# Optimization experiments

Measured on AMD Instinct MI355X. Metric: run time of the kernel, lower is better.

## Reference

```python
import jax, jax.numpy as jnp
import numpy as np


def setup_inputs() -> dict:
    key = jax.random.key(0)
    k1, k2, k3, k4, k5 = jax.random.split(key, 5)
    return {
        "d1": jax.random.normal(k1, (2, 4096, 512), dtype=jnp.float32),
        "d2": jax.random.normal(k2, (2, 512, 4096), dtype=jnp.float32),
        "d3": jax.random.normal(k3, (2, 4096, 512), dtype=jnp.float32),
        "d4": jax.random.normal(k4, (512, 512), dtype=jnp.float32),
        "d5": jax.random.normal(k5, (1, 512), dtype=jnp.float32),
    }


def reference(d1, d2, d3, d4, d5):
    # attention core: scores = d1 @ d2 -> [2, 4096, 4096]
    scores = jnp.einsum('bsd,bdt->bst', d1, d2)
    attn = jax.nn.softmax(scores, axis=2)
    # weighted values: [2, 4096, 512]
    ctx = jnp.einsum('bst,btd->bsd', attn, d3)
    # flatten batch*seq and apply final projection with bias (addmm)
    x = ctx.reshape(8192, 512)
    return d5 + x @ d4  # d5 [1,512] broadcasts over rows
```

## Files before the change

### kernel.cpp

```cpp
#include <hip/hip_runtime.h>

typedef unsigned short u16;
typedef __attribute__((ext_vector_type(8))) short short8;
typedef __attribute__((ext_vector_type(4))) float f32x4;

#define MFMA16(a, b, c) __builtin_amdgcn_mfma_f32_16x16x32_bf16((a), (b), (c), 0, 0, 0)
#define ASYNC_CP16(g, l)                                                        \
  __builtin_amdgcn_global_load_lds((const __attribute__((address_space(1))) void*)(g), \
                                   (__attribute__((address_space(3))) void*)(l), 16, 0, 0)

constexpr int Bb = 2, Ss = 4096, Tt = 4096, Dd = 512;
constexpr int BM = 64, BN = 64, TP = 4;
constexpr int TPART = Tt / TP;
constexpr int TCH = TPART / BN;

constexpr size_t SZ_BF = (size_t)Bb * Ss * Dd * 2;
constexpr size_t O_QH   = 0;
constexpr size_t O_QL   = O_QH + SZ_BF;
constexpr size_t O_D2TH = O_QL + SZ_BF;
constexpr size_t O_D2TL = O_D2TH + SZ_BF;
constexpr size_t O_D3T  = O_D2TL + SZ_BF;
constexpr size_t O_D4T  = O_D3T + SZ_BF;
constexpr size_t O_CTX  = O_D4T + (size_t)512 * 512 * 2;
constexpr size_t O_OP   = O_CTX + SZ_BF;
constexpr size_t O_MP   = O_OP + (size_t)TP * SZ_BF;
constexpr size_t O_LP   = O_MP + (size_t)TP * Bb * Ss * 4;

__device__ __forceinline__ u16 f2bf(float x) {
  union { float f; unsigned u; } v; v.f = x;
  unsigned r = v.u + 0x7fffu + ((v.u >> 16) & 1u);
  return (u16)(r >> 16);
}
__device__ __forceinline__ float bf2f(u16 h) {
  union { unsigned u; float f; } v; v.u = ((unsigned)h) << 16;
  return v.f;
}

__device__ __forceinline__ void transpose_sp(const float* __restrict__ in,
                                             u16* __restrict__ outh,
                                             u16* __restrict__ outl, int R, int C,
                                             int bx, int by, int bz,
                                             int tx, int ty, float* tile) {
  const float* inb = in + (size_t)bz * R * C;
  const int x = bx * 32 + tx;
  const int y0 = by * 32;
  for (int j = ty; j < 32; j += 8)
    tile[j * 33 + tx] = inb[(size_t)(y0 + j) * C + x];
  __syncthreads();
  const size_t ob = (size_t)bz * C * R;
  for (int j = ty; j < 32; j += 8) {
    float v = tile[tx * 33 + j];
    size_t oi = ob + (size_t)(bx * 32 + j) * R + (y0 + tx);
    u16 h = f2bf(v);
    outh[oi] = h;
    if (outl) outl[oi] = f2bf(v - bf2f(h));
  }
}

__global__ void prep_kernel(const float* __restrict__ d1, const float* __restrict__ d2,
                            const float* __restrict__ d3, const float* __restrict__ d4,
                            u16* __restrict__ qh, u16* __restrict__ ql,
                            u16* __restrict__ d2th, u16* __restrict__ d2tl,
                            u16* __restrict__ d3t, u16* __restrict__ d4t) {
  __shared__ float tile[32 * 33];
  const int bid = blockIdx.x;
  const int tid = threadIdx.x;
  const int tx = tid & 31, ty = tid >> 5;
  if (bid < 4096) {
    const int i = bid * 256 + tid;
    float4 v = ((const float4*)d1)[i];
    ushort4 hh, ll;
    hh.x = f2bf(v.x); ll.x = f2bf(v.x - bf2f(hh.x));
    hh.y = f2bf(v.y); ll.y = f2bf(v.y - bf2f(hh.y));
    hh.z = f2bf(v.z); ll.z = f2bf(v.z - bf2f(hh.z));
    hh.w = f2bf(v.w); ll.w = f2bf(v.w - bf2f(hh.w));
    ((ushort4*)qh)[i] = hh;
    ((ushort4*)ql)[i] = ll;
  } else if (bid < 8192) {
    const int t = bid - 4096;
    transpose_sp(d2, d2th, d2tl, 512, 4096, t & 127, (t >> 7) & 15, t >> 11, tx, ty, tile);
  } else if (bid < 12288) {
    const int t = bid - 8192;
    transpose_sp(d3, d3t, nullptr, 4096, 512, t & 15, (t >> 4) & 127, t >> 11, tx, ty, tile);
  } else {
    const int t = bid - 12288;
    transpose_sp(d4, d4t, nullptr, 512, 512, t & 15, t >> 4, 0, tx, ty, tile);
  }
}

__global__ __launch_bounds__(256, 2)
void flash_part_kernel(const u16* __restrict__ qh_g,
                       const u16* __restrict__ ql_g,
                       const u16* __restrict__ d2th,
                       const u16* __restrict__ d2tl,
                       const u16* __restrict__ d3t,
                       u16* __restrict__ opart,
                       float* __restrict__ mpart,
                       float* __restrict__ lpart) {
  __shared__ u16 bufs[2][16384];
  __shared__ u16 ph[64 * 72];

  const int tid = threadIdx.x;
  const int wave = tid >> 6, lane = tid & 63, quad = lane >> 4, l15 = lane & 15;
  const int m0 = wave * 16;
  const int s0 = blockIdx.x * BM, tp = blockIdx.y, b = blockIdx.z;

  f32x4 o_acc[32];
#pragma unroll
  for (int i = 0; i < 32; i++) o_acc[i] = (f32x4){0.f, 0.f, 0.f, 0.f};
  f32x4 s_acc[4];
  float m_r[4] = {-INFINITY, -INFINITY, -INFINITY, -INFINITY};
  float l_r[4] = {0.f, 0.f, 0.f, 0.f};

  const u16* qh_row = qh_g + ((size_t)b * Ss + s0 + m0 + l15) * Dd + quad * 8;
  const u16* ql_row = ql_g + ((size_t)b * Ss + s0 + m0 + l15) * Dd + quad * 8;
  const u16* kh_b = d2th + (size_t)b * Tt * Dd;
  const u16* kl_b = d2tl + (size_t)b * Tt * Dd;
  const u16* v_b  = d3t  + (size_t)b * Dd * Tt;

  const int l4 = lane >> 4;
  const int cb16 = lane & 15;
  const int vr8 = lane >> 3;
  const int vcb = (lane & 7) ^ (vr8 & 7);

  {
    const int t0 = tp * TPART;
#pragma unroll
    for (int u = 0; u < 4; u++) {
      const int rloc = wave * 16 + u * 4 + l4;
      const int gb = cb16 ^ (u * 4 + l4);
      const u16* sh = kh_b + (size_t)(t0 + rloc) * Dd + gb * 8;
      const u16* sl = kl_b + (size_t)(t0 + rloc) * Dd + gb * 8;
      u16* ld = &bufs[0][(wave * 16 + u * 4) * 128];
      ASYNC_CP16(sh, ld);
      ASYNC_CP16(sl, ld + 8192);
    }
  }
  __syncthreads();

  for (int tc = 0; tc < TCH; tc++) {
#pragma unroll
    for (int sub = 0; sub < 8; sub++) {
      const bool has_next = (sub < 7) || (tc < TCH - 1);
      const int nsub = (sub + 1) & 7;
      const int ntc = (sub == 7) ? tc + 1 : tc;

      if (has_next) {
        const int nt0 = tp * TPART + ntc * BN;
        u16* nb = bufs[nsub & 1];
        if (nsub < 4) {
          const int d0 = nsub * 128;
#pragma unroll
          for (int u = 0; u < 4; u++) {
            const int rloc = wave * 16 + u * 4 + l4;
            const int gb = cb16 ^ (u * 4 + l4);
            const u16* sh = kh_b + (size_t)(nt0 + rloc) * Dd + d0 + gb * 8;
            const u16* sl = kl_b + (size_t)(nt0 + rloc) * Dd + d0 + gb * 8;
            u16* ld = &nb[(wave * 16 + u * 4) * 128];
            ASYNC_CP16(sh, ld);
            ASYNC_CP16(sl, ld + 8192);
          }
        } else {
          const int nc = nsub - 4;
#pragma unroll
          for (int u = 0; u < 4; u++) {
            const int rloc = wave * 32 + u * 8 + vr8;
            const u16* sv = v_b + (size_t)(nc * 128 + rloc) * Tt + nt0 + vcb * 8;
            u16* ld = &nb[(wave * 32 + u * 8) * 64];
            ASYNC_CP16(sv, ld);
          }
        }
      }

      const u16* bb = bufs[sub & 1];
      if (sub < 4) {
        if (sub == 0) {
#pragma unroll
          for (int nt = 0; nt < 4; nt++) s_acc[nt] = (f32x4){0.f, 0.f, 0.f, 0.f};
        }
        const int d0 = sub * 128;
        short8 ah[4], al[4];
#pragma unroll
        for (int ks = 0; ks < 4; ks++) {
          ah[ks] = *(const short8*)(qh_row + d0 + ks * 32);
          al[ks] = *(const short8*)(ql_row + d0 + ks * 32);
        }
#pragma unroll
        for (int ks = 0; ks < 4; ks++) {
#pragma unroll
          for (int nt = 0; nt < 4; nt++) {
            const int rr = nt * 16 + l15;
            const int off = rr * 128 + (((ks * 4 + quad) ^ l15)) * 8;
            short8 bh = *(const short8*)&bb[off];
            short8 bl = *(const short8*)&bb[8192 + off];
            s_acc[nt] = MFMA16(ah[ks], bh, s_acc[nt]);
            s_acc[nt] = MFMA16(al[ks], bh, s_acc[nt]);
            s_acc[nt] = MFMA16(ah[ks], bl, s_acc[nt]);
          }
        }
        if (sub == 3) {
          float alpha[4], psum[4];
#pragma unroll
          for (int r = 0; r < 4; r++) {
            float v = fmaxf(fmaxf(s_acc[0][r], s_acc[1][r]), fmaxf(s_acc[2][r], s_acc[3][r]));
            v = fmaxf(v, __shfl_xor(v, 1));
            v = fmaxf(v, __shfl_xor(v, 2));
            v = fmaxf(v, __shfl_xor(v, 4));
            v = fmaxf(v, __shfl_xor(v, 8));
            float mn = fmaxf(m_r[r], v);
            alpha[r] = __expf(m_r[r] - mn);
            m_r[r] = mn;
            psum[r] = 0.f;
          }
#pragma unroll
          for (int nt = 0; nt < 4; nt++) {
#pragma unroll
            for (int r = 0; r < 4; r++) {
              float p = __expf(s_acc[nt][r] - m_r[r]);
              psum[r] += p;
              ph[(m0 + quad * 4 + r) * 72 + nt * 16 + l15] = f2bf(p);
            }
          }
#pragma unroll
          for (int r = 0; r < 4; r++) {
            float v = psum[r];
            v += __shfl_xor(v, 1);
            v += __shfl_xor(v, 2);
            v += __shfl_xor(v, 4);
            v += __shfl_xor(v, 8);
            l_r[r] = l_r[r] * alpha[r] + v;
          }
          bool need = (alpha[0] != 1.f) | (alpha[1] != 1.f) | (alpha[2] != 1.f) | (alpha[3] != 1.f);
          if (__any(need)) {
#pragma unroll
            for (int j = 0; j < 32; j++)
#pragma unroll
              for (int r = 0; r < 4; r++) o_acc[j][r] *= alpha[r];
          }
        }
      } else {
        const int nc = sub - 4;
#pragma unroll
        for (int ks = 0; ks < 2; ks++) {
          const int kk = ks * 32 + quad * 8;
          short8 ap = *(const short8*)&ph[(m0 + l15) * 72 + kk];
#pragma unroll
          for (int nt = 0; nt < 8; nt++) {
            const int rr = nt * 16 + l15;
            const int off = rr * 64 + (((ks * 4 + quad) ^ (l15 & 7))) * 8;
            short8 bv = *(const short8*)&bb[off];
            o_acc[nc * 8 + nt] = MFMA16(ap, bv, o_acc[nc * 8 + nt]);
          }
        }
      }

      __syncthreads();
    }
  }

  const size_t obase = (((size_t)tp * Bb + b) * Ss + s0) * Dd;
#pragma unroll
  for (int j = 0; j < 32; j++) {
    const int col = (j >> 3) * 128 + (j & 7) * 16 + l15;
#pragma unroll
    for (int r = 0; r < 4; r++) {
      const int row = m0 + quad * 4 + r;
      opart[obase + (size_t)row * Dd + col] = f2bf(o_acc[j][r]);
    }
  }
  if (l15 == 0) {
    const size_t sbase = ((size_t)tp * Bb + b) * Ss + s0;
#pragma unroll
    for (int r = 0; r < 4; r++) {
      const int row = m0 + quad * 4 + r;
      mpart[sbase + row] = m_r[r];
      lpart[sbase + row] = l_r[r];
    }
  }
}

__global__ void combine_kernel(const u16* __restrict__ opart,
                               const float* __restrict__ mpart,
                               const float* __restrict__ lpart,
                               u16* __restrict__ ctx) {
  const int idx = blockIdx.x * blockDim.x + threadIdx.x;
  const int vpr = Dd / 8;
  const int row = idx / vpr;
  const int dv = (idx % vpr) * 8;
  float mv[TP], mM = -INFINITY;
#pragma unroll
  for (int p = 0; p < TP; p++) {
    mv[p] = mpart[(size_t)p * Bb * Ss + row];
    mM = fmaxf(mM, mv[p]);
  }
  float w[TP], denom = 0.f;
#pragma unroll
  for (int p = 0; p < TP; p++) {
    float e = __expf(mv[p] - mM);
    w[p] = e;
    denom += e * lpart[(size_t)p * Bb * Ss + row];
  }
  const float inv = 1.0f / denom;
  float acc[8];
#pragma unroll
  for (int e = 0; e < 8; e++) acc[e] = 0.f;
#pragma unroll
  for (int p = 0; p < TP; p++) {
    uint4 raw = *(const uint4*)&opart[(size_t)p * Bb * Ss * Dd + (size_t)row * Dd + dv];
    const u16* u = (const u16*)&raw;
#pragma unroll
    for (int e = 0; e < 8; e++) acc[e] += w[p] * bf2f(u[e]);
  }
  u16 outv[8];
#pragma unroll
  for (int e = 0; e < 8; e++) outv[e] = f2bf(acc[e] * inv);
  *(uint4*)&ctx[(size_t)row * Dd + dv] = *(const uint4*)outv;
}

__global__ __launch_bounds__(256, 2)
void proj_kernel(const u16* __restrict__ ctx,
                 const u16* __restrict__ d4t,
                 const float* __restrict__ d5,
                 float* __restrict__ out) {
  __shared__ u16 a_lds[128 * 40], b_lds[128 * 40];
  const int tid = threadIdx.x;
  const int wave = tid >> 6, lane = tid & 63, quad = lane >> 4, l15 = lane & 15;
  const int m0w = (wave & 1) * 64, n0w = (wave >> 1) * 64;
  const int bm = blockIdx.x, bn = blockIdx.y;
  f32x4 acc[4][4];
#pragma unroll
  for (int i = 0; i < 4; i++)
#pragma unroll
    for (int j = 0; j < 4; j++) acc[i][j] = (f32x4){0.f, 0.f, 0.f, 0.f};

  const int srow = tid >> 2, scol = (tid & 3) * 8;
  for (int kt = 0; kt < 16; kt++) {
    const int k0 = kt * 32;
    __syncthreads();
#pragma unroll
    for (int pass = 0; pass < 2; pass++) {
      const int row = srow + pass * 64;
      *(uint4*)&a_lds[row * 40 + scol] =
          *(const uint4*)&ctx[(size_t)(bm * 128 + row) * Dd + k0 + scol];
      *(uint4*)&b_lds[row * 40 + scol] =
          *(const uint4*)&d4t[(size_t)(bn * 128 + row) * Dd + k0 + scol];
    }
    __syncthreads();
    short8 af[4], bfr[4];
#pragma unroll
    for (int i = 0; i < 4; i++)
      af[i] = *(const short8*)&a_lds[(m0w + 16 * i + l15) * 40 + quad * 8];
#pragma unroll
    for (int j = 0; j < 4; j++)
      bfr[j] = *(const short8*)&b_lds[(n0w + 16 * j + l15) * 40 + quad * 8];
#pragma unroll
    for (int i = 0; i < 4; i++)
#pragma unroll
      for (int j = 0; j < 4; j++) acc[i][j] = MFMA16(af[i], bfr[j], acc[i][j]);
  }
#pragma unroll
  for (int j = 0; j < 4; j++) {
    const int colg = bn * 128 + n0w + 16 * j + l15;
    const float bias = d5[colg];
#pragma unroll
    for (int i = 0; i < 4; i++) {
#pragma unroll
      for (int r = 0; r < 4; r++) {
        const int rowg = bm * 128 + m0w + 16 * i + quad * 4 + r;
        out[(size_t)rowg * 512 + colg] = acc[i][j][r] + bias;
      }
    }
  }
}

extern "C" void kernel_launch(void* const* d_in, const int* in_sizes, int n_in,
                              void* d_out, int out_size, void* d_ws, size_t ws_size,
                              hipStream_t stream) {
  (void)in_sizes; (void)n_in; (void)out_size; (void)ws_size;
  const float* d1 = (const float*)d_in[0];
  const float* d2 = (const float*)d_in[1];
  const float* d3 = (const float*)d_in[2];
  const float* d4 = (const float*)d_in[3];
  const float* d5 = (const float*)d_in[4];
  float* out = (float*)d_out;
  char* ws = (char*)d_ws;

  u16* qh_g = (u16*)(ws + O_QH);
  u16* ql_g = (u16*)(ws + O_QL);
  u16* d2th = (u16*)(ws + O_D2TH);
  u16* d2tl = (u16*)(ws + O_D2TL);
  u16* d3t  = (u16*)(ws + O_D3T);
  u16* d4t  = (u16*)(ws + O_D4T);
  u16* ctx  = (u16*)(ws + O_CTX);
  u16* opart = (u16*)(ws + O_OP);
  float* mpart = (float*)(ws + O_MP);
  float* lpart = (float*)(ws + O_LP);

  prep_kernel<<<12544, 256, 0, stream>>>(d1, d2, d3, d4, qh_g, ql_g, d2th, d2tl, d3t, d4t);
  flash_part_kernel<<<dim3(Ss / BM, TP, Bb), 256, 0, stream>>>(qh_g, ql_g, d2th, d2tl, d3t,
                                                               opart, mpart, lpart);
  combine_kernel<<<(Bb * Ss * Dd / 8) / 256, 256, 0, stream>>>(opart, mpart, lpart, ctx);
  proj_kernel<<<dim3(64, 4), 256, 0, stream>>>(ctx, d4t, d5, out);
}
```

Before: 555.7 us.

## Double query tile to 128 rows with 8 waves and hoist Q fragments into registers

The flash attention partial kernel now uses 128 query rows per block with 512 threads. Each staged K/V tile in shared memory is therefore shared by twice as many waves, and each wave issues half as many async copies. The query hi/lo fragments for all of D are loaded once into registers instead of being re-read from global memory on every chunk. The grid is reordered so the T-partition and batch are the fast index. This costs many more registers per thread (32 extra short8 values on top of 32 f32x4 accumulators), which risks spilling or lower occupancy at launch bounds of 512 threads and 2 blocks, and it halves the number of blocks.

```diff
diff --git a/kernel.cpp b/kernel.cpp
--- a/kernel.cpp
+++ b/kernel.cpp
@@ -10,7 +10,7 @@
                                    (__attribute__((address_space(3))) void*)(l), 16, 0, 0)
 
 constexpr int Bb = 2, Ss = 4096, Tt = 4096, Dd = 512;
-constexpr int BM = 64, BN = 64, TP = 4;
+constexpr int BM = 128, BN = 64, TP = 4;
 constexpr int TPART = Tt / TP;
 constexpr int TCH = TPART / BN;
 
@@ -88,7 +88,7 @@
   }
 }
 
-__global__ __launch_bounds__(256, 2)
+__global__ __launch_bounds__(512, 2)
 void flash_part_kernel(const u16* __restrict__ qh_g,
                        const u16* __restrict__ ql_g,
                        const u16* __restrict__ d2th,
@@ -98,12 +98,13 @@
                        float* __restrict__ mpart,
                        float* __restrict__ lpart) {
   __shared__ u16 bufs[2][16384];
-  __shared__ u16 ph[64 * 72];
+  __shared__ u16 ph[128 * 72];
 
   const int tid = threadIdx.x;
   const int wave = tid >> 6, lane = tid & 63, quad = lane >> 4, l15 = lane & 15;
   const int m0 = wave * 16;
-  const int s0 = blockIdx.x * BM, tp = blockIdx.y, b = blockIdx.z;
+  const int tp = blockIdx.x & 3, b = blockIdx.x >> 2;
+  const int s0 = blockIdx.y * BM;
 
   f32x4 o_acc[32];
 #pragma unroll
@@ -112,11 +113,22 @@
   float m_r[4] = {-INFINITY, -INFINITY, -INFINITY, -INFINITY};
   float l_r[4] = {0.f, 0.f, 0.f, 0.f};
 
-  const u16* qh_row = qh_g + ((size_t)b * Ss + s0 + m0 + l15) * Dd + quad * 8;
-  const u16* ql_row = ql_g + ((size_t)b * Ss + s0 + m0 + l15) * Dd + quad * 8;
   const u16* kh_b = d2th + (size_t)b * Tt * Dd;
   const u16* kl_b = d2tl + (size_t)b * Tt * Dd;
   const u16* v_b  = d3t  + (size_t)b * Dd * Tt;
+
+  short8 qf_h[4][4], qf_l[4][4];
+  {
+    const u16* qh_row = qh_g + ((size_t)b * Ss + s0 + m0 + l15) * Dd + quad * 8;
+    const u16* ql_row = ql_g + ((size_t)b * Ss + s0 + m0 + l15) * Dd + quad * 8;
+#pragma unroll
+    for (int sub = 0; sub < 4; sub++)
+#pragma unroll
+      for (int ks = 0; ks < 4; ks++) {
+        qf_h[sub][ks] = *(const short8*)(qh_row + sub * 128 + ks * 32);
+        qf_l[sub][ks] = *(const short8*)(ql_row + sub * 128 + ks * 32);
+      }
+  }
 
   const int l4 = lane >> 4;
   const int cb16 = lane & 15;
@@ -126,12 +138,13 @@
   {
     const int t0 = tp * TPART;
 #pragma unroll
-    for (int u = 0; u < 4; u++) {
-      const int rloc = wave * 16 + u * 4 + l4;
-      const int gb = cb16 ^ (u * 4 + l4);
+    for (int u = 0; u < 2; u++) {
+      const int rbase = wave * 8 + u * 4;
+      const int rloc = rbase + l4;
+      const int gb = cb16 ^ (rloc & 15);
       const u16* sh = kh_b + (size_t)(t0 + rloc) * Dd + gb * 8;
       const u16* sl = kl_b + (size_t)(t0 + rloc) * Dd + gb * 8;
-      u16* ld = &bufs[0][(wave * 16 + u * 4) * 128];
+      u16* ld = &bufs[0][rbase * 128];
       ASYNC_CP16(sh, ld);
       ASYNC_CP16(sl, ld + 8192);
     }
@@ -151,22 +164,24 @@
         if (nsub < 4) {
           const int d0 = nsub * 128;
 #pragma unroll
-          for (int u = 0; u < 4; u++) {
-            const int rloc = wave * 16 + u * 4 + l4;
-            const int gb = cb16 ^ (u * 4 + l4);
+          for (int u = 0; u < 2; u++) {
+            const int rbase = wave * 8 + u * 4;
+            const int rloc = rbase + l4;
+            const int gb = cb16 ^ (rloc & 15);
             const u16* sh = kh_b + (size_t)(nt0 + rloc) * Dd + d0 + gb * 8;
             const u16* sl = kl_b + (size_t)(nt0 + rloc) * Dd + d0 + gb * 8;
-            u16* ld = &nb[(wave * 16 + u * 4) * 128];
+            u16* ld = &nb[rbase * 128];
             ASYNC_CP16(sh, ld);
             ASYNC_CP16(sl, ld + 8192);
           }
         } else {
           const int nc = nsub - 4;
 #pragma unroll
-          for (int u = 0; u < 4; u++) {
-            const int rloc = wave * 32 + u * 8 + vr8;
+          for (int u = 0; u < 2; u++) {
+            const int rbase = wave * 16 + u * 8;
+            const int rloc = rbase + vr8;
             const u16* sv = v_b + (size_t)(nc * 128 + rloc) * Tt + nt0 + vcb * 8;
-            u16* ld = &nb[(wave * 32 + u * 8) * 64];
+            u16* ld = &nb[rbase * 64];
             ASYNC_CP16(sv, ld);
           }
         }
@@ -177,13 +192,6 @@
         if (sub == 0) {
 #pragma unroll
           for (int nt = 0; nt < 4; nt++) s_acc[nt] = (f32x4){0.f, 0.f, 0.f, 0.f};
-        }
-        const int d0 = sub * 128;
-        short8 ah[4], al[4];
-#pragma unroll
-        for (int ks = 0; ks < 4; ks++) {
-          ah[ks] = *(const short8*)(qh_row + d0 + ks * 32);
-          al[ks] = *(const short8*)(ql_row + d0 + ks * 32);
         }
 #pragma unroll
         for (int ks = 0; ks < 4; ks++) {
@@ -193,9 +201,9 @@
             const int off = rr * 128 + (((ks * 4 + quad) ^ l15)) * 8;
             short8 bh = *(const short8*)&bb[off];
             short8 bl = *(const short8*)&bb[8192 + off];
-            s_acc[nt] = MFMA16(ah[ks], bh, s_acc[nt]);
-            s_acc[nt] = MFMA16(al[ks], bh, s_acc[nt]);
-            s_acc[nt] = MFMA16(ah[ks], bl, s_acc[nt]);
+            s_acc[nt] = MFMA16(qf_h[sub][ks], bh, s_acc[nt]);
+            s_acc[nt] = MFMA16(qf_l[sub][ks], bh, s_acc[nt]);
+            s_acc[nt] = MFMA16(qf_h[sub][ks], bl, s_acc[nt]);
           }
         }
         if (sub == 3) {
@@ -397,8 +405,8 @@
   float* lpart = (float*)(ws + O_LP);
 
   prep_kernel<<<12544, 256, 0, stream>>>(d1, d2, d3, d4, qh_g, ql_g, d2th, d2tl, d3t, d4t);
-  flash_part_kernel<<<dim3(Ss / BM, TP, Bb), 256, 0, stream>>>(qh_g, ql_g, d2th, d2tl, d3t,
-                                                               opart, mpart, lpart);
+  flash_part_kernel<<<dim3(8, 32), 512, 0, stream>>>(qh_g, ql_g, d2th, d2tl, d3t,
+                                                     opart, mpart, lpart);
   combine_kernel<<<(Bb * Ss * Dd / 8) / 256, 256, 0, stream>>>(opart, mpart, lpart, ctx);
   proj_kernel<<<dim3(64, 4), 256, 0, stream>>>(ctx, d4t, d5, out);
 }
```

Result: no change. 552.7 us (-0.5%).
